# Optimization experiments

Hardware: AMD Instinct MI355X
Metric: run time of the kernel (lower is better)

Reference implementation:

```python
import jax, jax.numpy as jnp
import numpy as np

N = 50000
E = 800000
G = 2500  # number of graphs


def setup_inputs() -> dict:
    key = jax.random.key(0)
    ks = jax.random.split(key, 10)
    x = jax.random.normal(ks[0], (N, 128), dtype=jnp.float32)
    edge_index = jax.random.randint(ks[1], (2, E), 0, N, dtype=jnp.int64)
    batch = jnp.sort(jax.random.randint(ks[2], (N,), 0, G, dtype=jnp.int64))
    def lin(k, fan_in, shape):
        return jax.random.normal(k, shape, dtype=jnp.float32) / np.sqrt(fan_in)
    return {
        'x': x, 'edge_index': edge_index, 'batch': batch,
        'W1': lin(ks[3], 128, (128, 64)), 'b1': jnp.zeros((64,), jnp.float32),
        'W2': lin(ks[4], 64, (64, 64)),  'b2': jnp.zeros((64,), jnp.float32),
        'W3': lin(ks[5], 64, (64, 64)),  'b3': jnp.zeros((64,), jnp.float32),
        'Wp1': lin(ks[6], 64, (64, 64)), 'bp1': jnp.zeros((64,), jnp.float32),
        'Wp2': lin(ks[7], 64, (64, 32)), 'bp2': jnp.zeros((32,), jnp.float32),
    }


def _gcn_norm(edge_index, n_nodes):
    # PyG GCNConv default: add self-loops, symmetric normalization
    loops = jnp.arange(n_nodes, dtype=edge_index.dtype)
    src = jnp.concatenate([edge_index[0], loops])
    dst = jnp.concatenate([edge_index[1], loops])
    deg = jax.ops.segment_sum(jnp.ones_like(dst, dtype=jnp.float32), dst,
                              num_segments=n_nodes)
    dis = jnp.where(deg > 0, jax.lax.rsqrt(deg), 0.0)
    norm = dis[src] * dis[dst]  # [E + N]
    return src, dst, norm


def _gcn_conv(x, W, b, src, dst, norm, n_nodes):
    h = x @ W                                   # transform first (small dim)
    m = h[src] * norm[:, None]                  # gather + scale
    out = jax.ops.segment_sum(m, dst, num_segments=n_nodes)  # scatter-add
    return out + b


def reference(x, edge_index, batch, W1, b1, W2, b2, W3, b3, Wp1, bp1, Wp2, bp2):
    n_nodes = x.shape[0]
    src, dst, norm = _gcn_norm(edge_index, n_nodes)
    x1 = jax.nn.relu(_gcn_conv(x, W1, b1, src, dst, norm, n_nodes))
    x2 = jax.nn.relu(_gcn_conv(x1, W2, b2, src, dst, norm, n_nodes))
    x3 = jax.nn.relu(_gcn_conv(x2, W3, b3, src, dst, norm, n_nodes))
    h = x1 + x2 + x3
    # global_mean_pool
    sums = jax.ops.segment_sum(h, batch, num_segments=G)
    counts = jax.ops.segment_sum(jnp.ones((n_nodes,), jnp.float32), batch,
                                 num_segments=G)
    pooled = sums / jnp.maximum(counts, 1.0)[:, None]
    z = jax.nn.relu(pooled @ Wp1 + bp1) @ Wp2 + bp2
    return z
```

## Files before the change

### kernel.cpp

```cpp
#include <hip/hip_runtime.h>
#include <math.h>


typedef short short8 __attribute__((ext_vector_type(8)));
typedef float f32x4 __attribute__((ext_vector_type(4)));

__device__ inline float bf2f(unsigned short h) {
    return __uint_as_float((unsigned)h << 16);
}
__device__ inline unsigned short f2bf(float f) {
    unsigned u = __float_as_uint(f);
    return (unsigned short)((u + (0x7FFFu + ((u >> 16) & 1u))) >> 16);
}
__device__ inline unsigned short f2h(float f) {
    union { _Float16 h; unsigned short u; } c;
    c.h = (_Float16)f;
    return c.u;
}
__device__ inline float h2f(unsigned short u) {
    union { unsigned short u; _Float16 h; } c;
    c.u = u;
    return (float)c.h;
}
__device__ inline void bh8f(short8 u, float4& a, float4& b) {
    a.x = bf2f((unsigned short)u[0]); a.y = bf2f((unsigned short)u[1]);
    a.z = bf2f((unsigned short)u[2]); a.w = bf2f((unsigned short)u[3]);
    b.x = bf2f((unsigned short)u[4]); b.y = bf2f((unsigned short)u[5]);
    b.z = bf2f((unsigned short)u[6]); b.w = bf2f((unsigned short)u[7]);
}
__device__ inline float4 f4fma(float s, float4 a, float4 acc) {
    acc.x += s * a.x; acc.y += s * a.y; acc.z += s * a.z; acc.w += s * a.w;
    return acc;
}

template <int K>
__global__ __launch_bounds__(256) void k_hist_gemm(const int* __restrict__ dst,
                                                   int* __restrict__ hist, int E, int chunk,
                                                   const float* __restrict__ X,
                                                   const float* __restrict__ W,
                                                   unsigned short* __restrict__ H, int n) {
    __shared__ int hh[256];
    __shared__ short wt[64 * K];
    int t = threadIdx.x;
    if (blockIdx.x < 256) {
        hh[t] = 0;
        __syncthreads();
        int e0 = blockIdx.x * chunk;
        int e1 = min(e0 + chunk, E);
        for (int e = e0 + t; e < e1; e += 256) atomicAdd(&hh[dst[e] >> 8], 1);
        __syncthreads();
        hist[blockIdx.x * 256 + t] = hh[t];
        return;
    }
    for (int idx = t; idx < 64 * K; idx += 256) {
        int k = idx >> 6, ch = idx & 63;
        wt[ch * K + k] = (short)f2bf(W[idx]);
    }
    __syncthreads();
    int wave = t >> 6, lane = t & 63;
    int q = lane >> 4, l = lane & 15;
    int tile = (blockIdx.x - 256) * 4 + wave;
    if (tile * 16 >= n) return;
    int node = tile * 16 + l;
    short8 afr[4][K / 32];
#pragma unroll
    for (int mb = 0; mb < 4; mb++)
#pragma unroll
        for (int s = 0; s < K / 32; s++)
            afr[mb][s] = *(const short8*)(wt + (mb * 16 + l) * K + s * 32 + q * 8);
    f32x4 acc[4] = {};
    const float* xr = X + (size_t)node * K + q * 8;
#pragma unroll
    for (int s = 0; s < K / 32; s++) {
        float4 xa = *(const float4*)(xr + s * 32);
        float4 xb = *(const float4*)(xr + s * 32 + 4);
        short8 bfr;
        bfr[0] = (short)f2bf(xa.x); bfr[1] = (short)f2bf(xa.y);
        bfr[2] = (short)f2bf(xa.z); bfr[3] = (short)f2bf(xa.w);
        bfr[4] = (short)f2bf(xb.x); bfr[5] = (short)f2bf(xb.y);
        bfr[6] = (short)f2bf(xb.z); bfr[7] = (short)f2bf(xb.w);
#pragma unroll
        for (int mb = 0; mb < 4; mb++)
            acc[mb] = __builtin_amdgcn_mfma_f32_16x16x32_bf16(afr[mb][s], bfr, acc[mb], 0, 0, 0);
    }
#pragma unroll
    for (int mb = 0; mb < 4; mb++) {
        ushort4 u;
        u.x = f2bf(acc[mb][0]); u.y = f2bf(acc[mb][1]);
        u.z = f2bf(acc[mb][2]); u.w = f2bf(acc[mb][3]);
        ((ushort4*)H)[(size_t)node * 16 + mb * 4 + q] = u;
    }
}

__global__ void kA_colscan(const int* __restrict__ hist, int* __restrict__ cursorA,
                           int* __restrict__ tot) {
    __shared__ int s[256];
    int t = threadIdx.x;
    int k = blockIdx.x;
    int v = hist[t * 256 + k];
    s[t] = v;
    __syncthreads();
    for (int st = 1; st < 256; st <<= 1) {
        int u = s[t];
        if (t >= st) u += s[t - st];
        __syncthreads();
        s[t] = u;
        __syncthreads();
    }
    cursorA[t * 256 + k] = s[t] - v;
    if (t == 255) tot[k] = s[255];
}

__global__ void kA_scatter(const int* __restrict__ src, const int* __restrict__ dst,
                           const int* __restrict__ cursorA, const int* __restrict__ tot,
                           unsigned* __restrict__ ebuf, int E, int chunk) {
    __shared__ int s[256];
    __shared__ int cur[256];
    int t = threadIdx.x;
    s[t] = tot[t];
    __syncthreads();
    for (int st = 1; st < 256; st <<= 1) {
        int u = s[t];
        if (t >= st) u += s[t - st];
        __syncthreads();
        s[t] = u;
        __syncthreads();
    }
    int bstart = (t == 0) ? 0 : s[t - 1];
    cur[t] = cursorA[blockIdx.x * 256 + t] + bstart;
    __syncthreads();
    int e0 = blockIdx.x * chunk;
    int e1 = min(e0 + chunk, E);
    for (int e = e0 + t; e < e1; e += 256) {
        int d = dst[e];
        int p = atomicAdd(&cur[d >> 8], 1);
        ebuf[p] = ((unsigned)(d & 255) << 24) | (unsigned)src[e];
    }
}

__global__ void kB1(const unsigned* __restrict__ ebuf, const int* __restrict__ tot,
                    float* __restrict__ dis, int* __restrict__ offsP, int N) {
    __shared__ int s[256];
    __shared__ int h[256];
    int t = threadIdx.x;
    int k = blockIdx.x;
    s[t] = tot[t];
    __syncthreads();
    for (int st = 1; st < 256; st <<= 1) {
        int u = s[t];
        if (t >= st) u += s[t - st];
        __syncthreads();
        s[t] = u;
        __syncthreads();
    }
    int lo = (k == 0) ? 0 : s[k - 1];
    int hi = s[k];
    int padbase = lo + 768 * k;
    h[t] = 0;
    __syncthreads();
    for (int p = lo + t; p < hi; p += 256) atomicAdd(&h[ebuf[p] >> 24], 1);
    __syncthreads();
    int c = h[t];
    int cp = (c + 3) & ~3;
    int node = k * 256 + t;
    if (node < N) dis[node] = rsqrtf((float)(c + 1));
    s[t] = cp;
    __syncthreads();
    for (int st = 1; st < 256; st <<= 1) {
        int u = s[t];
        if (t >= st) u += s[t - st];
        __syncthreads();
        s[t] = u;
        __syncthreads();
    }
    if (node < N) offsP[node] = ((padbase + s[t] - cp) << 9) | cp;
}

__global__ void kB2(const unsigned* __restrict__ ebuf, const int* __restrict__ tot,
                    const float* __restrict__ dis, const int* __restrict__ offsP,
                    unsigned* __restrict__ col, int N) {
    __shared__ int s[256];
    __shared__ int cur[256];
    int t = threadIdx.x;
    int k = blockIdx.x;
    s[t] = tot[t];
    __syncthreads();
    for (int st = 1; st < 256; st <<= 1) {
        int u = s[t];
        if (t >= st) u += s[t - st];
        __syncthreads();
        s[t] = u;
        __syncthreads();
    }
    int lo = (k == 0) ? 0 : s[k - 1];
    int hi = s[k];
    int node = k * 256 + t;
    int po = (node < N) ? offsP[node] : 0;
    cur[t] = po >> 9;
    __syncthreads();
    for (int p = lo + t; p < hi; p += 256) {
        unsigned e = ebuf[p];
        int srcI = (int)(e & 0x00FFFFFFu);
        int q = atomicAdd(&cur[e >> 24], 1);
        col[q] = ((unsigned)f2h(dis[srcI]) << 16) | (unsigned)srcI;
    }
    __syncthreads();
    if (node < N) {
        int end = (po >> 9) + (po & 511);
        for (int q = cur[t]; q < end; q++) col[q] = 0u;
    }
}

__global__ __launch_bounds__(256) void k_aggemm(const unsigned short* __restrict__ H,
                                                const unsigned* __restrict__ col,
                                                const int* __restrict__ offsP,
                                                const float* __restrict__ dis,
                                                const float* __restrict__ bias,
                                                const float* __restrict__ W,
                                                unsigned short* __restrict__ Xout,
                                                unsigned short* __restrict__ Hout, int n) {
    __shared__ short wt[64 * 64];
    __shared__ short vbuf[64 * 72];
    int t = threadIdx.x;
    for (int idx = t; idx < 64 * 64; idx += 256) {
        int k = idx >> 6, ch = idx & 63;
        wt[ch * 64 + k] = (short)f2bf(W[idx]);
    }
    const short8* Hs = (const short8*)H;
    int base = blockIdx.x * 64;
    int cs = t & 7;
    const float4* bias4 = (const float4*)bias;
    float4 bb0 = bias4[cs * 2];
    float4 bb1 = bias4[cs * 2 + 1];
#pragma unroll
    for (int r = 0; r < 2; r++) {
        int nl = r * 32 + (t >> 3);
        int node = base + nl;
        if (node < n) {
            float dn = dis[node];
            float4 acc0, acc1;
            bh8f(Hs[(size_t)node * 8 + cs], acc0, acc1);
            acc0.x *= dn; acc0.y *= dn; acc0.z *= dn; acc0.w *= dn;
            acc1.x *= dn; acc1.y *= dn; acc1.z *= dn; acc1.w *= dn;
            int po = offsP[node];
            int p = po >> 9, hi = p + (po & 511);
            for (; p < hi; p += 4) {
                uint4 e4 = *(const uint4*)(col + p);
                short8 g0 = Hs[(size_t)(e4.x & 0xFFFFu) * 8 + cs];
                short8 g1 = Hs[(size_t)(e4.y & 0xFFFFu) * 8 + cs];
                short8 g2 = Hs[(size_t)(e4.z & 0xFFFFu) * 8 + cs];
                short8 g3 = Hs[(size_t)(e4.w & 0xFFFFu) * 8 + cs];
                float w0 = h2f((unsigned short)(e4.x >> 16));
                float w1 = h2f((unsigned short)(e4.y >> 16));
                float w2 = h2f((unsigned short)(e4.z >> 16));
                float w3 = h2f((unsigned short)(e4.w >> 16));
                float4 a, b;
                bh8f(g0, a, b); acc0 = f4fma(w0, a, acc0); acc1 = f4fma(w0, b, acc1);
                bh8f(g1, a, b); acc0 = f4fma(w1, a, acc0); acc1 = f4fma(w1, b, acc1);
                bh8f(g2, a, b); acc0 = f4fma(w2, a, acc0); acc1 = f4fma(w2, b, acc1);
                bh8f(g3, a, b); acc0 = f4fma(w3, a, acc0); acc1 = f4fma(w3, b, acc1);
            }
            float4 v0, v1;
            v0.x = fmaxf(acc0.x * dn + bb0.x, 0.f);
            v0.y = fmaxf(acc0.y * dn + bb0.y, 0.f);
            v0.z = fmaxf(acc0.z * dn + bb0.z, 0.f);
            v0.w = fmaxf(acc0.w * dn + bb0.w, 0.f);
            v1.x = fmaxf(acc1.x * dn + bb1.x, 0.f);
            v1.y = fmaxf(acc1.y * dn + bb1.y, 0.f);
            v1.z = fmaxf(acc1.z * dn + bb1.z, 0.f);
            v1.w = fmaxf(acc1.w * dn + bb1.w, 0.f);
            short8 o;
            o[0] = (short)f2bf(v0.x); o[1] = (short)f2bf(v0.y);
            o[2] = (short)f2bf(v0.z); o[3] = (short)f2bf(v0.w);
            o[4] = (short)f2bf(v1.x); o[5] = (short)f2bf(v1.y);
            o[6] = (short)f2bf(v1.z); o[7] = (short)f2bf(v1.w);
            ((short8*)Xout)[(size_t)node * 8 + cs] = o;
            *(short8*)(vbuf + nl * 72 + cs * 8) = o;
        }
    }
    __syncthreads();
    int wave = t >> 6, lane = t & 63;
    int q = lane >> 4, l = lane & 15;
    if (base + wave * 16 >= n) return;
    int node = base + wave * 16 + l;
    short8 afr[4][2];
#pragma unroll
    for (int mb = 0; mb < 4; mb++)
#pragma unroll
        for (int s = 0; s < 2; s++)
            afr[mb][s] = *(const short8*)(wt + (mb * 16 + l) * 64 + s * 32 + q * 8);
    f32x4 acc[4] = {};
#pragma unroll
    for (int s = 0; s < 2; s++) {
        short8 bfr = *(const short8*)(vbuf + (wave * 16 + l) * 72 + s * 32 + q * 8);
#pragma unroll
        for (int mb = 0; mb < 4; mb++)
            acc[mb] = __builtin_amdgcn_mfma_f32_16x16x32_bf16(afr[mb][s], bfr, acc[mb], 0, 0, 0);
    }
#pragma unroll
    for (int mb = 0; mb < 4; mb++) {
        ushort4 u;
        u.x = f2bf(acc[mb][0]); u.y = f2bf(acc[mb][1]);
        u.z = f2bf(acc[mb][2]); u.w = f2bf(acc[mb][3]);
        ((ushort4*)Hout)[(size_t)node * 16 + mb * 4 + q] = u;
    }
}

__global__ void k_agg3(const unsigned short* __restrict__ H, const unsigned* __restrict__ col,
                       const int* __restrict__ offsP, const float* __restrict__ dis,
                       const float* __restrict__ bias,
                       const unsigned short* __restrict__ add1,
                       const unsigned short* __restrict__ add2,
                       float* __restrict__ OutS, int n) {
    int t = threadIdx.x;
    int node = blockIdx.x * 32 + (t >> 3);
    if (node >= n) return;
    int lane = t & 7;
    const short8* Hs = (const short8*)H;
    float dn = dis[node];
    float4 acc0, acc1;
    bh8f(Hs[(size_t)node * 8 + lane], acc0, acc1);
    acc0.x *= dn; acc0.y *= dn; acc0.z *= dn; acc0.w *= dn;
    acc1.x *= dn; acc1.y *= dn; acc1.z *= dn; acc1.w *= dn;
    int po = offsP[node];
    int p = po >> 9, hi = p + (po & 511);
    for (; p < hi; p += 4) {
        uint4 e4 = *(const uint4*)(col + p);
        short8 g0 = Hs[(size_t)(e4.x & 0xFFFFu) * 8 + lane];
        short8 g1 = Hs[(size_t)(e4.y & 0xFFFFu) * 8 + lane];
        short8 g2 = Hs[(size_t)(e4.z & 0xFFFFu) * 8 + lane];
        short8 g3 = Hs[(size_t)(e4.w & 0xFFFFu) * 8 + lane];
        float w0 = h2f((unsigned short)(e4.x >> 16));
        float w1 = h2f((unsigned short)(e4.y >> 16));
        float w2 = h2f((unsigned short)(e4.z >> 16));
        float w3 = h2f((unsigned short)(e4.w >> 16));
        float4 a, b;
        bh8f(g0, a, b); acc0 = f4fma(w0, a, acc0); acc1 = f4fma(w0, b, acc1);
        bh8f(g1, a, b); acc0 = f4fma(w1, a, acc0); acc1 = f4fma(w1, b, acc1);
        bh8f(g2, a, b); acc0 = f4fma(w2, a, acc0); acc1 = f4fma(w2, b, acc1);
        bh8f(g3, a, b); acc0 = f4fma(w3, a, acc0); acc1 = f4fma(w3, b, acc1);
    }
    const float4* bias4 = (const float4*)bias;
    float4 bb0 = bias4[lane * 2];
    float4 bb1 = bias4[lane * 2 + 1];
    float4 v0, v1;
    v0.x = fmaxf(acc0.x * dn + bb0.x, 0.f);
    v0.y = fmaxf(acc0.y * dn + bb0.y, 0.f);
    v0.z = fmaxf(acc0.z * dn + bb0.z, 0.f);
    v0.w = fmaxf(acc0.w * dn + bb0.w, 0.f);
    v1.x = fmaxf(acc1.x * dn + bb1.x, 0.f);
    v1.y = fmaxf(acc1.y * dn + bb1.y, 0.f);
    v1.z = fmaxf(acc1.z * dn + bb1.z, 0.f);
    v1.w = fmaxf(acc1.w * dn + bb1.w, 0.f);
    size_t slot = (size_t)node * 8 + lane;
    float4 a10, a11, a20, a21;
    bh8f(((const short8*)add1)[slot], a10, a11);
    bh8f(((const short8*)add2)[slot], a20, a21);
    v0.x += a10.x + a20.x; v0.y += a10.y + a20.y;
    v0.z += a10.z + a20.z; v0.w += a10.w + a20.w;
    v1.x += a11.x + a21.x; v1.y += a11.y + a21.y;
    v1.z += a11.z + a21.z; v1.w += a11.w + a21.w;
    float4* S4 = (float4*)OutS;
    size_t oi = (size_t)node * 16 + (size_t)lane * 2;
    S4[oi] = v0;
    S4[oi + 1] = v1;
}

__global__ void k_poolhead(const float* __restrict__ S, const int* __restrict__ batch,
                           const float* __restrict__ Wp1, const float* __restrict__ bp1,
                           const float* __restrict__ Wp2, const float* __restrict__ bp2,
                           float* __restrict__ out, int n, int G) {
    int g = blockIdx.x;
    int j = threadIdx.x;
    int a = 0, b = n;
    while (a < b) { int m = (a + b) >> 1; if (batch[m] < g) a = m + 1; else b = m; }
    int beg = a;
    b = n;
    while (a < b) { int m = (a + b) >> 1; if (batch[m] < g + 1) a = m + 1; else b = m; }
    int end = a;
    float sum = 0.f;
    int i = beg;
    for (; i + 2 <= end; i += 2)
        sum += S[(size_t)i * 64 + j] + S[(size_t)(i + 1) * 64 + j];
    if (i < end) sum += S[(size_t)i * 64 + j];
    float cnt = (float)(end - beg);
    float p = sum / fmaxf(cnt, 1.f);
    __shared__ float ps[64];
    __shared__ float ts[64];
    ps[j] = p;
    __syncthreads();
    float t1 = bp1[j];
#pragma unroll 8
    for (int k = 0; k < 64; k++) t1 += ps[k] * Wp1[k * 64 + j];
    t1 = fmaxf(t1, 0.f);
    ts[j] = t1;
    __syncthreads();
    if (j < 32) {
        float o = bp2[j];
#pragma unroll 8
        for (int k = 0; k < 64; k++) o += ts[k] * Wp2[k * 32 + j];
        out[(size_t)g * 32 + j] = o;
    }
}

extern "C" void kernel_launch(void* const* d_in, const int* in_sizes, int n_in,
                              void* d_out, int out_size, void* d_ws, size_t ws_size,
                              hipStream_t stream) {
    const float* x   = (const float*)d_in[0];
    const int*   ei  = (const int*)d_in[1];
    const int*   bat = (const int*)d_in[2];
    const float* W1  = (const float*)d_in[3];
    const float* b1  = (const float*)d_in[4];
    const float* W2  = (const float*)d_in[5];
    const float* b2  = (const float*)d_in[6];
    const float* W3  = (const float*)d_in[7];
    const float* b3  = (const float*)d_in[8];
    const float* Wp1 = (const float*)d_in[9];
    const float* bp1 = (const float*)d_in[10];
    const float* Wp2 = (const float*)d_in[11];
    const float* bp2 = (const float*)d_in[12];

    int N = in_sizes[0] / 128;
    int E = in_sizes[1] / 2;
    int G = out_size / 32;
    const int* src = ei;
    const int* dst = ei + E;

    char* w = (char*)d_ws;
    auto alloc = [&](size_t bytes) -> void* {
        void* p = (void*)w;
        w += (bytes + 255) & ~(size_t)255;
        return p;
    };
    int NB = (N + 255) / 256;
    int*            offsP   = (int*)alloc((size_t)N * 4);
    unsigned*       col     = (unsigned*)alloc(((size_t)E + 3 * (size_t)N + 1024) * 4);
    float*          dis     = (float*)alloc((size_t)N * 4);
    int*            hist    = (int*)alloc((size_t)256 * 256 * 4);
    int*            cursorA = (int*)alloc((size_t)256 * 256 * 4);
    int*            tot     = (int*)alloc((size_t)256 * 4);
    unsigned*       ebuf    = (unsigned*)alloc((size_t)E * 4);
    unsigned short* Hb      = (unsigned short*)alloc((size_t)N * 64 * 2);
    unsigned short* Hb2     = (unsigned short*)alloc((size_t)N * 64 * 2);
    unsigned short* X1      = (unsigned short*)alloc((size_t)N * 64 * 2);
    unsigned short* X2      = (unsigned short*)alloc((size_t)N * 64 * 2);
    float*          S       = (float*)alloc((size_t)N * 64 * 4);

    int chunk = (E + 255) / 256;
    int ggemm = ((N >> 4) + 3) / 4;
    int gfuse = (N + 63) / 64;
    int gagg  = (N + 31) / 32;

    k_hist_gemm<128><<<256 + ggemm, 256, 0, stream>>>(dst, hist, E, chunk, x, W1, Hb, N);
    kA_colscan<<<256, 256, 0, stream>>>(hist, cursorA, tot);
    kA_scatter<<<256, 256, 0, stream>>>(src, dst, cursorA, tot, ebuf, E, chunk);
    kB1<<<NB, 256, 0, stream>>>(ebuf, tot, dis, offsP, N);
    kB2<<<NB, 256, 0, stream>>>(ebuf, tot, dis, offsP, col, N);

    k_aggemm<<<gfuse, 256, 0, stream>>>(Hb, col, offsP, dis, b1, W2, X1, Hb2, N);
    k_aggemm<<<gfuse, 256, 0, stream>>>(Hb2, col, offsP, dis, b2, W3, X2, Hb, N);
    k_agg3<<<gagg, 256, 0, stream>>>(Hb, col, offsP, dis, b3, X1, X2, S, N);

    k_poolhead<<<G, 64, 0, stream>>>(S, bat, Wp1, bp1, Wp2, bp2, (float*)d_out, N, G);
}
```

Measured before the change: 222.8 us.

## Prescale features by source norm, drop per-edge weights, fuse mean-pool via atomics

Folds the source-side degree normalization into the stored feature rows: layer 1 is rescaled in the merged kB kernel, and later GEMMs multiply by dis before storing. Edge lists now hold plain source indices, so aggregation becomes unweighted adds with no fp16 weight decode. kB1 and kB2 are merged into one kernel, padding entries point at a zeroed dummy row instead of node 0, and the final aggregation atomically accumulates into per-graph pooled sums. This removes the large S buffer and the pooling read pass, at the cost of many float atomics on contended graph rows and an extra read-modify-write pass over Hb.

```diff
diff --git a/kernel.cpp b/kernel.cpp
--- a/kernel.cpp
+++ b/kernel.cpp
@@ -11,16 +11,6 @@
 __device__ inline unsigned short f2bf(float f) {
     unsigned u = __float_as_uint(f);
     return (unsigned short)((u + (0x7FFFu + ((u >> 16) & 1u))) >> 16);
-}
-__device__ inline unsigned short f2h(float f) {
-    union { _Float16 h; unsigned short u; } c;
-    c.h = (_Float16)f;
-    return c.u;
-}
-__device__ inline float h2f(unsigned short u) {
-    union { unsigned short u; _Float16 h; } c;
-    c.u = u;
-    return (float)c.h;
 }
 __device__ inline void bh8f(short8 u, float4& a, float4& b) {
     a.x = bf2f((unsigned short)u[0]); a.y = bf2f((unsigned short)u[1]);
@@ -28,8 +18,8 @@
     b.x = bf2f((unsigned short)u[4]); b.y = bf2f((unsigned short)u[5]);
     b.z = bf2f((unsigned short)u[6]); b.w = bf2f((unsigned short)u[7]);
 }
-__device__ inline float4 f4fma(float s, float4 a, float4 acc) {
-    acc.x += s * a.x; acc.y += s * a.y; acc.z += s * a.z; acc.w += s * a.w;
+__device__ inline float4 f4add(float4 a, float4 acc) {
+    acc.x += a.x; acc.y += a.y; acc.z += a.z; acc.w += a.w;
     return acc;
 }
 
@@ -93,7 +83,7 @@
 }
 
 __global__ void kA_colscan(const int* __restrict__ hist, int* __restrict__ cursorA,
-                           int* __restrict__ tot) {
+                           int* __restrict__ tot, float* __restrict__ pooled, int PG) {
     __shared__ int s[256];
     int t = threadIdx.x;
     int k = blockIdx.x;
@@ -109,6 +99,7 @@
     }
     cursorA[t * 256 + k] = s[t] - v;
     if (t == 255) tot[k] = s[255];
+    for (int i = k * 256 + t; i < PG; i += 65536) pooled[i] = 0.f;
 }
 
 __global__ void kA_scatter(const int* __restrict__ src, const int* __restrict__ dst,
@@ -138,10 +129,14 @@
     }
 }
 
-__global__ void kB1(const unsigned* __restrict__ ebuf, const int* __restrict__ tot,
-                    float* __restrict__ dis, int* __restrict__ offsP, int N) {
+__global__ void kB(const unsigned* __restrict__ ebuf, const int* __restrict__ tot,
+                   float* __restrict__ dis, int* __restrict__ offsP,
+                   unsigned* __restrict__ col, unsigned short* __restrict__ Hb,
+                   unsigned short* __restrict__ Hb2, int N, int ZR) {
     __shared__ int s[256];
     __shared__ int h[256];
+    __shared__ int cur[256];
+    __shared__ float sdis[256];
     int t = threadIdx.x;
     int k = blockIdx.x;
     s[t] = tot[t];
@@ -155,7 +150,7 @@
     }
     int lo = (k == 0) ? 0 : s[k - 1];
     int hi = s[k];
-    int padbase = lo + 768 * k;
+    int padbase = ((lo + 3) & ~3) + 768 * k;
     h[t] = 0;
     __syncthreads();
     for (int p = lo + t; p < hi; p += 256) atomicAdd(&h[ebuf[p] >> 24], 1);
@@ -163,7 +158,9 @@
     int c = h[t];
     int cp = (c + 3) & ~3;
     int node = k * 256 + t;
-    if (node < N) dis[node] = rsqrtf((float)(c + 1));
+    float dn = rsqrtf((float)(c + 1));
+    sdis[t] = dn;
+    if (node < N) dis[node] = dn;
     s[t] = cp;
     __syncthreads();
     for (int st = 1; st < 256; st <<= 1) {
@@ -173,41 +170,38 @@
         s[t] = u;
         __syncthreads();
     }
-    if (node < N) offsP[node] = ((padbase + s[t] - cp) << 9) | cp;
-}
-
-__global__ void kB2(const unsigned* __restrict__ ebuf, const int* __restrict__ tot,
-                    const float* __restrict__ dis, const int* __restrict__ offsP,
-                    unsigned* __restrict__ col, int N) {
-    __shared__ int s[256];
-    __shared__ int cur[256];
-    int t = threadIdx.x;
-    int k = blockIdx.x;
-    s[t] = tot[t];
-    __syncthreads();
-    for (int st = 1; st < 256; st <<= 1) {
-        int u = s[t];
-        if (t >= st) u += s[t - st];
-        __syncthreads();
-        s[t] = u;
-        __syncthreads();
-    }
-    int lo = (k == 0) ? 0 : s[k - 1];
-    int hi = s[k];
-    int node = k * 256 + t;
-    int po = (node < N) ? offsP[node] : 0;
-    cur[t] = po >> 9;
+    int start = padbase + s[t] - cp;
+    if (node < N) offsP[node] = (start << 9) | cp;
+    cur[t] = start;
     __syncthreads();
     for (int p = lo + t; p < hi; p += 256) {
         unsigned e = ebuf[p];
-        int srcI = (int)(e & 0x00FFFFFFu);
         int q = atomicAdd(&cur[e >> 24], 1);
-        col[q] = ((unsigned)f2h(dis[srcI]) << 16) | (unsigned)srcI;
+        col[q] = e & 0x00FFFFFFu;
     }
     __syncthreads();
     if (node < N) {
-        int end = (po >> 9) + (po & 511);
-        for (int q = cur[t]; q < end; q++) col[q] = 0u;
+        int end = start + cp;
+        for (int q = cur[t]; q < end; q++) col[q] = (unsigned)ZR;
+    }
+    for (int idx = t; idx < 2048; idx += 256) {
+        int nl = idx >> 3, cs = idx & 7;
+        int nd = k * 256 + nl;
+        if (nd >= N) continue;
+        float d2 = sdis[nl];
+        short8 v = ((const short8*)Hb)[(size_t)nd * 8 + cs];
+        float4 a, b;
+        bh8f(v, a, b);
+        short8 o;
+        o[0] = (short)f2bf(a.x * d2); o[1] = (short)f2bf(a.y * d2);
+        o[2] = (short)f2bf(a.z * d2); o[3] = (short)f2bf(a.w * d2);
+        o[4] = (short)f2bf(b.x * d2); o[5] = (short)f2bf(b.y * d2);
+        o[6] = (short)f2bf(b.z * d2); o[7] = (short)f2bf(b.w * d2);
+        ((short8*)Hb)[(size_t)nd * 8 + cs] = o;
+    }
+    if (k == 0) {
+        if (t < 32) ((unsigned*)Hb)[(size_t)ZR * 32 + t] = 0u;
+        else if (t < 64) ((unsigned*)Hb2)[(size_t)ZR * 32 + (t - 32)] = 0u;
     }
 }
 
@@ -240,25 +234,19 @@
             float dn = dis[node];
             float4 acc0, acc1;
             bh8f(Hs[(size_t)node * 8 + cs], acc0, acc1);
-            acc0.x *= dn; acc0.y *= dn; acc0.z *= dn; acc0.w *= dn;
-            acc1.x *= dn; acc1.y *= dn; acc1.z *= dn; acc1.w *= dn;
             int po = offsP[node];
             int p = po >> 9, hi = p + (po & 511);
             for (; p < hi; p += 4) {
                 uint4 e4 = *(const uint4*)(col + p);
-                short8 g0 = Hs[(size_t)(e4.x & 0xFFFFu) * 8 + cs];
-                short8 g1 = Hs[(size_t)(e4.y & 0xFFFFu) * 8 + cs];
-                short8 g2 = Hs[(size_t)(e4.z & 0xFFFFu) * 8 + cs];
-                short8 g3 = Hs[(size_t)(e4.w & 0xFFFFu) * 8 + cs];
-                float w0 = h2f((unsigned short)(e4.x >> 16));
-                float w1 = h2f((unsigned short)(e4.y >> 16));
-                float w2 = h2f((unsigned short)(e4.z >> 16));
-                float w3 = h2f((unsigned short)(e4.w >> 16));
+                short8 g0 = Hs[(size_t)e4.x * 8 + cs];
+                short8 g1 = Hs[(size_t)e4.y * 8 + cs];
+                short8 g2 = Hs[(size_t)e4.z * 8 + cs];
+                short8 g3 = Hs[(size_t)e4.w * 8 + cs];
                 float4 a, b;
-                bh8f(g0, a, b); acc0 = f4fma(w0, a, acc0); acc1 = f4fma(w0, b, acc1);
-                bh8f(g1, a, b); acc0 = f4fma(w1, a, acc0); acc1 = f4fma(w1, b, acc1);
-                bh8f(g2, a, b); acc0 = f4fma(w2, a, acc0); acc1 = f4fma(w2, b, acc1);
-                bh8f(g3, a, b); acc0 = f4fma(w3, a, acc0); acc1 = f4fma(w3, b, acc1);
+                bh8f(g0, a, b); acc0 = f4add(a, acc0); acc1 = f4add(b, acc1);
+                bh8f(g1, a, b); acc0 = f4add(a, acc0); acc1 = f4add(b, acc1);
+                bh8f(g2, a, b); acc0 = f4add(a, acc0); acc1 = f4add(b, acc1);
+                bh8f(g3, a, b); acc0 = f4add(a, acc0); acc1 = f4add(b, acc1);
             }
             float4 v0, v1;
             v0.x = fmaxf(acc0.x * dn + bb0.x, 0.f);
@@ -283,6 +271,7 @@
     int q = lane >> 4, l = lane & 15;
     if (base + wave * 16 >= n) return;
     int node = base + wave * 16 + l;
+    float dn2 = dis[node];
     short8 afr[4][2];
 #pragma unroll
     for (int mb = 0; mb < 4; mb++)
@@ -300,18 +289,20 @@
 #pragma unroll
     for (int mb = 0; mb < 4; mb++) {
         ushort4 u;
-        u.x = f2bf(acc[mb][0]); u.y = f2bf(acc[mb][1]);
-        u.z = f2bf(acc[mb][2]); u.w = f2bf(acc[mb][3]);
+        u.x = f2bf(acc[mb][0] * dn2); u.y = f2bf(acc[mb][1] * dn2);
+        u.z = f2bf(acc[mb][2] * dn2); u.w = f2bf(acc[mb][3] * dn2);
         ((ushort4*)Hout)[(size_t)node * 16 + mb * 4 + q] = u;
     }
 }
 
-__global__ void k_agg3(const unsigned short* __restrict__ H, const unsigned* __restrict__ col,
-                       const int* __restrict__ offsP, const float* __restrict__ dis,
-                       const float* __restrict__ bias,
-                       const unsigned short* __restrict__ add1,
-                       const unsigned short* __restrict__ add2,
-                       float* __restrict__ OutS, int n) {
+__global__ void k_agg3pool(const unsigned short* __restrict__ H,
+                           const unsigned* __restrict__ col,
+                           const int* __restrict__ offsP, const float* __restrict__ dis,
+                           const float* __restrict__ bias,
+                           const unsigned short* __restrict__ add1,
+                           const unsigned short* __restrict__ add2,
+                           const int* __restrict__ batch,
+                           float* __restrict__ pooled, int n) {
     int t = threadIdx.x;
     int node = blockIdx.x * 32 + (t >> 3);
     if (node >= n) return;
@@ -320,25 +311,19 @@
     float dn = dis[node];
     float4 acc0, acc1;
     bh8f(Hs[(size_t)node * 8 + lane], acc0, acc1);
-    acc0.x *= dn; acc0.y *= dn; acc0.z *= dn; acc0.w *= dn;
-    acc1.x *= dn; acc1.y *= dn; acc1.z *= dn; acc1.w *= dn;
     int po = offsP[node];
     int p = po >> 9, hi = p + (po & 511);
     for (; p < hi; p += 4) {
         uint4 e4 = *(const uint4*)(col + p);
-        short8 g0 = Hs[(size_t)(e4.x & 0xFFFFu) * 8 + lane];
-        short8 g1 = Hs[(size_t)(e4.y & 0xFFFFu) * 8 + lane];
-        short8 g2 = Hs[(size_t)(e4.z & 0xFFFFu) * 8 + lane];
-        short8 g3 = Hs[(size_t)(e4.w & 0xFFFFu) * 8 + lane];
-        float w0 = h2f((unsigned short)(e4.x >> 16));
-        float w1 = h2f((unsigned short)(e4.y >> 16));
-        float w2 = h2f((unsigned short)(e4.z >> 16));
-        float w3 = h2f((unsigned short)(e4.w >> 16));
+        short8 g0 = Hs[(size_t)e4.x * 8 + lane];
+        short8 g1 = Hs[(size_t)e4.y * 8 + lane];
+        short8 g2 = Hs[(size_t)e4.z * 8 + lane];
+        short8 g3 = Hs[(size_t)e4.w * 8 + lane];
         float4 a, b;
-        bh8f(g0, a, b); acc0 = f4fma(w0, a, acc0); acc1 = f4fma(w0, b, acc1);
-        bh8f(g1, a, b); acc0 = f4fma(w1, a, acc0); acc1 = f4fma(w1, b, acc1);
-        bh8f(g2, a, b); acc0 = f4fma(w2, a, acc0); acc1 = f4fma(w2, b, acc1);
-        bh8f(g3, a, b); acc0 = f4fma(w3, a, acc0); acc1 = f4fma(w3, b, acc1);
+        bh8f(g0, a, b); acc0 = f4add(a, acc0); acc1 = f4add(b, acc1);
+        bh8f(g1, a, b); acc0 = f4add(a, acc0); acc1 = f4add(b, acc1);
+        bh8f(g2, a, b); acc0 = f4add(a, acc0); acc1 = f4add(b, acc1);
+        bh8f(g3, a, b); acc0 = f4add(a, acc0); acc1 = f4add(b, acc1);
     }
     const float4* bias4 = (const float4*)bias;
     float4 bb0 = bias4[lane * 2];
@@ -360,16 +345,18 @@
     v0.z += a10.z + a20.z; v0.w += a10.w + a20.w;
     v1.x += a11.x + a21.x; v1.y += a11.y + a21.y;
     v1.z += a11.z + a21.z; v1.w += a11.w + a21.w;
-    float4* S4 = (float4*)OutS;
-    size_t oi = (size_t)node * 16 + (size_t)lane * 2;
-    S4[oi] = v0;
-    S4[oi + 1] = v1;
-}
-
-__global__ void k_poolhead(const float* __restrict__ S, const int* __restrict__ batch,
-                           const float* __restrict__ Wp1, const float* __restrict__ bp1,
-                           const float* __restrict__ Wp2, const float* __restrict__ bp2,
-                           float* __restrict__ out, int n, int G) {
+    int g = batch[node];
+    float* pr = pooled + (size_t)g * 64 + (size_t)lane * 8;
+    atomicAdd(pr + 0, v0.x); atomicAdd(pr + 1, v0.y);
+    atomicAdd(pr + 2, v0.z); atomicAdd(pr + 3, v0.w);
+    atomicAdd(pr + 4, v1.x); atomicAdd(pr + 5, v1.y);
+    atomicAdd(pr + 6, v1.z); atomicAdd(pr + 7, v1.w);
+}
+
+__global__ void k_head(const float* __restrict__ pooled, const int* __restrict__ batch,
+                       const float* __restrict__ Wp1, const float* __restrict__ bp1,
+                       const float* __restrict__ Wp2, const float* __restrict__ bp2,
+                       float* __restrict__ out, int n, int G) {
     int g = blockIdx.x;
     int j = threadIdx.x;
     int a = 0, b = n;
@@ -378,13 +365,8 @@
     b = n;
     while (a < b) { int m = (a + b) >> 1; if (batch[m] < g + 1) a = m + 1; else b = m; }
     int end = a;
-    float sum = 0.f;
-    int i = beg;
-    for (; i + 2 <= end; i += 2)
-        sum += S[(size_t)i * 64 + j] + S[(size_t)(i + 1) * 64 + j];
-    if (i < end) sum += S[(size_t)i * 64 + j];
     float cnt = (float)(end - beg);
-    float p = sum / fmaxf(cnt, 1.f);
+    float p = pooled[(size_t)g * 64 + j] / fmaxf(cnt, 1.f);
     __shared__ float ps[64];
     __shared__ float ts[64];
     ps[j] = p;
@@ -433,18 +415,19 @@
         return p;
     };
     int NB = (N + 255) / 256;
+    int ZR = N;
     int*            offsP   = (int*)alloc((size_t)N * 4);
-    unsigned*       col     = (unsigned*)alloc(((size_t)E + 3 * (size_t)N + 1024) * 4);
+    unsigned*       col     = (unsigned*)alloc(((size_t)E + 3 * (size_t)N + 2048) * 4);
     float*          dis     = (float*)alloc((size_t)N * 4);
     int*            hist    = (int*)alloc((size_t)256 * 256 * 4);
     int*            cursorA = (int*)alloc((size_t)256 * 256 * 4);
     int*            tot     = (int*)alloc((size_t)256 * 4);
     unsigned*       ebuf    = (unsigned*)alloc((size_t)E * 4);
-    unsigned short* Hb      = (unsigned short*)alloc((size_t)N * 64 * 2);
-    unsigned short* Hb2     = (unsigned short*)alloc((size_t)N * 64 * 2);
+    unsigned short* Hb      = (unsigned short*)alloc(((size_t)N + 16) * 64 * 2);
+    unsigned short* Hb2     = (unsigned short*)alloc(((size_t)N + 16) * 64 * 2);
     unsigned short* X1      = (unsigned short*)alloc((size_t)N * 64 * 2);
     unsigned short* X2      = (unsigned short*)alloc((size_t)N * 64 * 2);
-    float*          S       = (float*)alloc((size_t)N * 64 * 4);
+    float*          pooled  = (float*)alloc((size_t)G * 64 * 4);
 
     int chunk = (E + 255) / 256;
     int ggemm = ((N >> 4) + 3) / 4;
@@ -452,14 +435,13 @@
     int gagg  = (N + 31) / 32;
 
     k_hist_gemm<128><<<256 + ggemm, 256, 0, stream>>>(dst, hist, E, chunk, x, W1, Hb, N);
-    kA_colscan<<<256, 256, 0, stream>>>(hist, cursorA, tot);
+    kA_colscan<<<256, 256, 0, stream>>>(hist, cursorA, tot, pooled, G * 64);
     kA_scatter<<<256, 256, 0, stream>>>(src, dst, cursorA, tot, ebuf, E, chunk);
-    kB1<<<NB, 256, 0, stream>>>(ebuf, tot, dis, offsP, N);
-    kB2<<<NB, 256, 0, stream>>>(ebuf, tot, dis, offsP, col, N);
+    kB<<<NB, 256, 0, stream>>>(ebuf, tot, dis, offsP, col, Hb, Hb2, N, ZR);
 
     k_aggemm<<<gfuse, 256, 0, stream>>>(Hb, col, offsP, dis, b1, W2, X1, Hb2, N);
     k_aggemm<<<gfuse, 256, 0, stream>>>(Hb2, col, offsP, dis, b2, W3, X2, Hb, N);
-    k_agg3<<<gagg, 256, 0, stream>>>(Hb, col, offsP, dis, b3, X1, X2, S, N);
-
-    k_poolhead<<<G, 64, 0, stream>>>(S, bat, Wp1, bp1, Wp2, bp2, (float*)d_out, N, G);
-}
+    k_agg3pool<<<gagg, 256, 0, stream>>>(Hb, col, offsP, dis, b3, X1, X2, bat, pooled, N);
+
+    k_head<<<G, 64, 0, stream>>>(pooled, bat, Wp1, bp1, Wp2, bp2, (float*)d_out, N, G);
+}
```

Result: slower. 343.3 us (+54.1%).
